# Optimization experiments

Measured on AMD Instinct MI355X. Metric: run time of the kernel, lower is better.

Reference implementation:

```python
import jax, jax.numpy as jnp
import numpy as np

L, D, H, FFN, V = 24, 512, 16, 2048, 1025
HD = D // H
TOP_K = 15
REP_PEN = 1.35


def _layernorm(x, w, b, eps=1e-5):
    m = jnp.mean(x, -1, keepdims=True)
    var = jnp.var(x, -1, keepdims=True)
    return (x - m) / jnp.sqrt(var + eps) * w + b


def _sine_pe(T, d):
    pos = jnp.arange(T, dtype=jnp.float32)[:, None]
    div = jnp.exp(jnp.arange(0, d, 2, dtype=jnp.float32) * (-np.log(10000.0) / d))
    pe = jnp.zeros((T, d), jnp.float32)
    pe = pe.at[:, 0::2].set(jnp.sin(pos * div))
    pe = pe.at[:, 1::2].set(jnp.cos(pos * div))
    return pe


def setup_inputs():
    S, Ty, B = 2047, 1535, 1
    key = jax.random.key(0)
    ks = jax.random.split(key, 16)
    n = lambda i, sh, s=0.02: jax.random.normal(ks[i], sh, jnp.float32) * s
    return {
        "y": jax.random.randint(ks[0], (B, Ty + 1), 0, V, jnp.int32),
        "k": n(1, (L, S, B, D), 1.0),
        "v": n(2, (L, S, B, D), 1.0),
        "y_emb": n(3, (B, Ty, D), 1.0),
        "x_example": n(4, (B, 512), 1.0),
        "alpha": jnp.ones((1,), jnp.float32),
        "emb_table": n(5, (V, D)),
        "in_proj_w": n(6, (L, 3 * D, D)),
        "in_proj_b": jnp.zeros((L, 3 * D), jnp.float32),
        "out_w": n(7, (L, D, D)),
        "out_b": jnp.zeros((L, D), jnp.float32),
        "ln1_w": jnp.ones((L, D), jnp.float32),
        "ln1_b": jnp.zeros((L, D), jnp.float32),
        "ln2_w": jnp.ones((L, D), jnp.float32),
        "ln2_b": jnp.zeros((L, D), jnp.float32),
        "ffn_w1": n(8, (L, FFN, D)),
        "ffn_b1": jnp.zeros((L, FFN), jnp.float32),
        "ffn_w2": n(9, (L, D, FFN)),
        "ffn_b2": jnp.zeros((L, D), jnp.float32),
        "pred_w": n(10, (V, D)),
        "pred_b": jnp.zeros((V,), jnp.float32),
        "noise": jax.random.normal(ks[11], (V,), jnp.float32),
    }


def reference(y, k, v, y_emb, x_example, alpha, emb_table,
              in_proj_w, in_proj_b, out_w, out_b,
              ln1_w, ln1_b, ln2_w, ln2_b,
              ffn_w1, ffn_b1, ffn_w2, ffn_b2,
              pred_w, pred_b, noise):
    B = y.shape[0]
    # pad KV caches by one slot along seq dim (dim 1) -> [L, S+1, B, D]
    k_pad = jnp.pad(k, ((0, 0), (0, 1), (0, 0), (0, 0)))
    v_pad = jnp.pad(v, ((0, 0), (0, 1), (0, 0), (0, 0)))

    # embed newest token, extend y_emb cache
    new_emb = emb_table[y[:, -1:]]                       # [B,1,D]
    y_emb_new = jnp.concatenate([y_emb, new_emb], axis=1)  # [B,T,D]
    T = y_emb_new.shape[1]
    pe = _sine_pe(T, D)
    y_pos = y_emb_new + alpha * pe[None]                 # scale=False -> x_scale=1
    x = y_pos[:, -1:]                                    # [B,1,D] single query token

    scale = 1.0 / jnp.sqrt(jnp.float32(HD))

    def scan_body(x, per):
        kl, vl, wqkv, bqkv, wo, bo, g1, b1, g2, b2, fw1, fb1, fw2, fb2 = per
        qkv = jnp.einsum('bqd,ed->bqe', x, wqkv) + bqkv  # [B,1,3D]
        q, k_new, v_new = jnp.split(qkv, 3, axis=-1)
        kl = kl.at[-1].set(k_new[:, 0])                  # write into last cache slot
        vl = vl.at[-1].set(v_new[:, 0])
        qh = q.reshape(B, 1, H, HD)
        kh = kl.reshape(-1, B, H, HD)                    # [S+1,B,H,hd]
        vh = vl.reshape(-1, B, H, HD)
        scores = jnp.einsum('bqhd,sbhd->bhqs', qh, kh) * scale
        attn = jax.nn.softmax(scores, axis=-1)
        ctx = jnp.einsum('bhqs,sbhd->bqhd', attn, vh).reshape(B, 1, D)
        attn_out = jnp.einsum('bqd,ed->bqe', ctx, wo) + bo
        x = _layernorm(x + attn_out, g1, b1)             # post-LN (torch default)
        hdn = jax.nn.relu(jnp.einsum('bqd,fd->bqf', x, fw1) + fb1)
        ff = jnp.einsum('bqf,df->bqd', hdn, fw2) + fb2
        x = _layernorm(x + ff, g2, b2)
        return x, (kl, vl)

    x, (k_out, v_out) = jax.lax.scan(
        scan_body, x,
        (k_pad, v_pad, in_proj_w, in_proj_b, out_w, out_b,
         ln1_w, ln1_b, ln2_w, ln2_b, ffn_w1, ffn_b1, ffn_w2, ffn_b2))

    logits = jnp.einsum('bd,vd->bv', x[:, -1], pred_w) + pred_b  # [B,V]

    # ---- sampling on logits[0] ----
    lg = logits[0]
    prev = y[0]
    # repetition penalty (gather -> transform -> scatter; dup indices write same value)
    score = lg[prev]
    score = jnp.where(score < 0, score * REP_PEN, score / REP_PEN)
    lg = lg.at[prev].set(score)
    # top_p == 1.0 -> skipped; temperature == 1.0
    pivot = jax.lax.top_k(lg, TOP_K)[0][-1]
    lg = jnp.where(lg < pivot, -jnp.inf, lg)
    probs = jax.nn.softmax(lg)
    # faithful to source: argmax(probs / randn_like(probs))
    samples = jnp.argmax(probs / noise).astype(jnp.int32)[None, None]  # [1,1]
    y_new = jnp.concatenate([y, samples.astype(y.dtype)], axis=1)
    return y_new, k_out, v_out, y_emb_new, logits, samples
```

## Files before the change

### kernel.cpp

```cpp
#include <hip/hip_runtime.h>
#include <math.h>

#define LL 24
#define DD 512
#define HH 16
#define FFD 2048
#define VV 1025
#define SS 2047
#define TKV 2048
#define TYY 1535
#define NBLK 256
#define NT 512

constexpr size_t O_YNEW  = 0;
constexpr size_t O_KOUT  = 1537;
constexpr size_t O_VOUT  = O_KOUT + (size_t)LL*TKV*DD;
constexpr size_t O_YEMB  = O_VOUT + (size_t)LL*TKV*DD;
constexpr size_t O_LOGITS= O_YEMB + (size_t)(TYY+1)*DD;
constexpr size_t O_SAMP  = O_LOGITS + VV;

constexpr int W_FFA  = 0;
constexpr int W_WY   = 8192;
constexpr int W_PART = 16384;
constexpr int W_KN   = 25088;
constexpr int W_VN   = 25600;

struct P {
  const int* y; const float* k; const float* v; const float* yemb;
  const float* alpha; const float* emb;
  const float* ipw; const float* ipb; const float* ow; const float* ob;
  const float* l1w; const float* l1b; const float* l2w; const float* l2b;
  const float* f1w; const float* f1b; const float* f2w; const float* f2b;
  const float* pw; const float* pb; const float* noise;
  float* out; float* ws;
};

__device__ __forceinline__ float dot4(float4 a, float4 b){
  return a.x*b.x + a.y*b.y + a.z*b.z + a.w*b.w;
}
__device__ __forceinline__ float ldv(const float* pp){
  return __hip_atomic_load(pp, __ATOMIC_RELAXED, __HIP_MEMORY_SCOPE_AGENT);
}
__device__ __forceinline__ void stv(float* pp, float v){
  __hip_atomic_store(pp, v, __ATOMIC_RELAXED, __HIP_MEMORY_SCOPE_AGENT);
}
__device__ __forceinline__ unsigned ldu(const unsigned* pp){
  return __hip_atomic_load(pp, __ATOMIC_RELAXED, __HIP_MEMORY_SCOPE_AGENT);
}

__device__ __forceinline__ void lbar(){
  asm volatile("s_waitcnt lgkmcnt(0)" ::: "memory");
  __builtin_amdgcn_s_barrier();
  __builtin_amdgcn_sched_barrier(0);
}

__device__ __forceinline__ void barr_arrive(unsigned* flags, unsigned ph){
  asm volatile("s_waitcnt vmcnt(0) lgkmcnt(0)" ::: "memory");
  __builtin_amdgcn_s_barrier();
  __builtin_amdgcn_sched_barrier(0);
  if (threadIdx.x == 0)
    __hip_atomic_store(&flags[blockIdx.x*16], ph, __ATOMIC_RELAXED, __HIP_MEMORY_SCOPE_AGENT);
}
__device__ __forceinline__ void barr_wait(unsigned* flags, unsigned ph){
  const int t = threadIdx.x;
  if (t < 64){
    for (;;){
      int ok = 1;
      #pragma unroll
      for (int i=0;i<4;++i) ok &= (int)(ldu(&flags[(t*4+i)*16]) >= ph);
      if (__all(ok)) break;
    }
  }
  __builtin_amdgcn_s_barrier();
  asm volatile("" ::: "memory");
}
__device__ __forceinline__ void barr_wait_head(unsigned* flags, unsigned ph, int h){
  const int t = threadIdx.x;
  if (t < 64){
    for (;;){
      int ok = 1;
      if (t < 16) ok = (int)(ldu(&flags[(t*16 + h)*16]) >= ph);
      if (__all(ok)) break;
    }
  }
  __builtin_amdgcn_s_barrier();
  asm volatile("" ::: "memory");
}

__device__ __forceinline__ float2 bsum2(float a, float b2, float2* r8, int t){
  for (int off=32; off; off>>=1){ a += __shfl_xor(a, off); b2 += __shfl_xor(b2, off); }
  lbar();
  if ((t & 63) == 0) r8[t >> 6] = make_float2(a, b2);
  lbar();
  float2 s = r8[0];
  #pragma unroll
  for (int i=1;i<8;++i){ s.x += r8[i].x; s.y += r8[i].y; }
  return s;
}
__device__ __forceinline__ void ln512g(float r, float g, float bb,
                                       float* dst, float2* r8, int t)
{
  float2 s = bsum2(r, r*r, r8, t);
  float mean = s.x * (1.f/512.f);
  float var  = fmaxf(s.y * (1.f/512.f) - mean*mean, 0.f);
  dst[t] = (r - mean) * rsqrtf(var + 1e-5f) * g + bb;
}
__device__ __forceinline__ void bargmax(float v, int i, float* r8v, int* r8i,
                                        int t, float& ov, int& oi)
{
  for (int off=32; off; off>>=1){
    float v2 = __shfl_xor(v, off); int i2 = __shfl_xor(i, off);
    if (v2 > v || (v2 == v && i2 < i)){ v = v2; i = i2; }
  }
  lbar();
  if ((t & 63) == 0){ r8v[t>>6] = v; r8i[t>>6] = i; }
  lbar();
  ov = r8v[0]; oi = r8i[0];
  #pragma unroll
  for (int kk=1; kk<8; ++kk){
    float v2 = r8v[kk]; int i2 = r8i[kk];
    if (v2 > ov || (v2 == ov && i2 < oi)){ ov = v2; oi = i2; }
  }
}

struct RegsQ  { float4 w[8]; float b[4]; };
struct RegsKV { float4 k0,k1,v0,v1; };
struct RegsTl { float4 t0,t1; float bias; };
struct RegsLN { float g2,b2,fb2; };
struct RegsBC { float2 oww; float4 f1p0,f1p1,f2p0,f2p1;
                float g1,b1,obv,f1bv; };

__device__ __forceinline__ void issueQ(const P& p, int l, int h, int t, RegsQ& q){
  const int lane = t & 63, w = t >> 6;
  const float* Wb = p.ipw + (size_t)l*1536*DD;
  const float* Bb = p.ipb + (size_t)l*1536;
  #pragma unroll
  for (int pp=0; pp<4; ++pp){
    int row = h*32 + w + 8*pp;
    const float4* wr = (const float4*)(Wb + (size_t)row*DD);
    q.w[2*pp] = wr[lane]; q.w[2*pp+1] = wr[lane+64];
    q.b[pp] = Bb[row];
  }
}
__device__ __forceinline__ void issueL(const P& p, int b, int t, RegsQ& q){
  const int lane = t & 63, w = t >> 6;
  int row = (w < 4) ? b*4 + w : ((b == 255 && w == 4) ? 1024 : -1);
  if (row >= 0){
    const float4* wr = (const float4*)(p.pw + (size_t)row*DD);
    q.w[0] = wr[lane]; q.w[1] = wr[lane+64];
    q.b[0] = p.pb[row];
  }
}
__device__ __forceinline__ void issueKV(const P& p, int l, int h, int c, int t,
                                        RegsKV& kv){
  const float* kb = p.k + (size_t)l*SS*DD;
  const float* vb = p.v + (size_t)l*SS*DD;
  const int s0 = c*128;
  kv.k0 = kv.v0 = kv.k1 = kv.v1 = make_float4(0,0,0,0);
  {
    int row = t >> 3, c4 = (t & 7)*4, s = s0 + row;
    if (s < SS){
      kv.k0 = *(const float4*)&kb[(size_t)s*DD + h*32 + c4];
      kv.v0 = *(const float4*)&vb[(size_t)s*DD + h*32 + c4];
    }
  }
  {
    int idx = t + NT;
    int row = idx >> 3, c4 = (idx & 7)*4, s = s0 + row;
    if (s < SS){
      kv.k1 = *(const float4*)&kb[(size_t)s*DD + h*32 + c4];
      kv.v1 = *(const float4*)&vb[(size_t)s*DD + h*32 + c4];
    }
  }
}
__device__ __forceinline__ void issueTl(const P& p, int l, int h, int c, int t,
                                        RegsTl& tl){
  const int lane = t & 63, w = t >> 6;
  if (w < 4){
    int isv = w >> 1;
    int row = 512 + isv*512 + h*32 + c*2 + (w&1);
    const float4* wr = (const float4*)(p.ipw + (size_t)l*1536*DD + (size_t)row*DD);
    tl.t0 = wr[lane]; tl.t1 = wr[lane+64];
    tl.bias = p.ipb[(size_t)l*1536 + row];
  }
}
__device__ __forceinline__ void issueLN(const P& p, int l, int t, RegsLN& r){
  r.g2 = p.l2w[(size_t)l*DD + t];
  r.b2 = p.l2b[(size_t)l*DD + t];
  r.fb2= p.f2b[(size_t)l*DD + t];
}
__device__ __forceinline__ void issueBC(const P& p, int l, int b, int h, int c,
                                        int t, RegsBC& bc){
  const int lane = t & 63, w = t >> 6;
  bc.oww = *(const float2*)(p.ow + (size_t)l*DD*DD
            + (size_t)(c*32 + (t>>4))*DD + h*32 + (t&15)*2);
  {
    int f = b*8 + w;
    const float4* wr = (const float4*)(p.f1w + (size_t)l*FFD*DD + (size_t)f*DD);
    bc.f1p0 = wr[lane]; bc.f1p1 = wr[lane+64];
    bc.f1bv = p.f1b[(size_t)l*FFD + f];
  }
  {
    const float* wr = p.f2w + (size_t)l*DD*FFD + (size_t)t*FFD + b*8;
    bc.f2p0 = *(const float4*)wr;
    bc.f2p1 = *(const float4*)(wr+4);
  }
  bc.g1  = p.l1w[(size_t)l*DD + t];
  bc.b1  = p.l1b[(size_t)l*DD + t];
  bc.obv = p.ob[(size_t)l*DD + t];
}

__global__ __launch_bounds__(NT, 1) void mega_kernel(P p)
{
  __shared__ __align__(16) float S_kl[128*33];
  __shared__ __align__(16) float S_vl[128*33];
  __shared__ __align__(16) float S_x[512];
  __shared__ float S_ps[128];
  __shared__ float S_cacc[512];
  __shared__ float S_pb[544];
  __shared__ float S_q[32];
  __shared__ float S_kn[32];
  __shared__ float S_vn[32];
  __shared__ float S_ctx[32];
  __shared__ float S_scal[4];
  __shared__ float S_hdn[8];
  __shared__ float2 S_r82[8];
  __shared__ float S_r8v[8];
  __shared__ int   S_r8i[8];

  const int t = threadIdx.x, b = blockIdx.x;
  const int lane = t & 63, w = t >> 6;
  const int h = b & 15, c = b >> 4;
  unsigned* flags = (unsigned*)p.ws;
  float* wsd = p.ws + 4352;
  float* out = p.out;
  unsigned ph = 0;

  RegsQ q; RegsKV kv; RegsTl tl; RegsLN lnp; RegsBC bc;
  issueQ(p, 0, h, t, q);
  issueKV(p, 0, h, c, t, kv);
  issueTl(p, 0, h, c, t, tl);

  for (int l = 0; l < LL; ++l){
    float fs = 0.f;
    if (l > 0){
      const float* fb = wsd + W_FFA + (size_t)((l+1)&1)*4096;
      #pragma unroll
      for (int i=0;i<8;++i) fs += ldv(&fb[i*512 + t]);
    }
    issueBC(p, l, b, h, c, t, bc);

    if (l == 0){
      int tok = p.y[1535];
      float a0 = p.alpha[0];
      float ev = p.emb[(size_t)tok*DD + t];
      float ang = 1535.0f * expf((float)(2*(t>>1)) * (-9.210340371976184f/512.0f));
      float pe = (t & 1) ? cosf(ang) : sinf(ang);
      S_x[t] = ev + a0*pe;
      if (b == 0) for (int i=t;i<1536;i+=NT)
        __builtin_nontemporal_store((float)p.y[i], out + O_YNEW + i);
      if (b == 1)
        __builtin_nontemporal_store(ev, out + O_YEMB + (size_t)TYY*DD + t);
      lbar();
    } else {
      float r = S_x[t] + lnp.fb2 + fs;
      ln512g(r, lnp.g2, lnp.b2, S_x, S_r82, t);
      lbar();
    }

    #pragma unroll
    for (int pp=0; pp<4; ++pp){
      float s = dot4(q.w[2*pp],   ((const float4*)S_x)[lane])
              + dot4(q.w[2*pp+1], ((const float4*)S_x)[lane+64]);
      for (int off=32; off; off>>=1) s += __shfl_xor(s, off);
      if (lane == 0) S_q[w + 8*pp] = s + q.b[pp];
    }
    if (w < 4){
      int isv = w >> 1;
      int col = h*32 + c*2 + (w & 1);
      float s = dot4(tl.t0, ((const float4*)S_x)[lane])
              + dot4(tl.t1, ((const float4*)S_x)[lane+64]);
      for (int off=32; off; off>>=1) s += __shfl_xor(s, off);
      if (lane == 0){
        float val = s + tl.bias;
        stv(&wsd[(isv ? W_VN : W_KN) + col], val);
        __builtin_nontemporal_store(val,
          out + (isv ? O_VOUT : O_KOUT) + (size_t)l*TKV*DD + (size_t)SS*DD + col);
      }
    }
    {
      int r0 = t >> 3, c40 = (t & 7)*4;
      int lb = r0*33 + c40;
      S_kl[lb+0]=kv.k0.x; S_kl[lb+1]=kv.k0.y; S_kl[lb+2]=kv.k0.z; S_kl[lb+3]=kv.k0.w;
      S_vl[lb+0]=kv.v0.x; S_vl[lb+1]=kv.v0.y; S_vl[lb+2]=kv.v0.z; S_vl[lb+3]=kv.v0.w;
      int idx = t + NT;
      int r1 = idx >> 3, c41 = (idx & 7)*4;
      int lb1 = r1*33 + c41;
      S_kl[lb1+0]=kv.k1.x; S_kl[lb1+1]=kv.k1.y; S_kl[lb1+2]=kv.k1.z; S_kl[lb1+3]=kv.k1.w;
      S_vl[lb1+0]=kv.v1.x; S_vl[lb1+1]=kv.v1.y; S_vl[lb1+2]=kv.v1.z; S_vl[lb1+3]=kv.v1.w;
    }
    lbar();

    {
      const int s0 = c*128;
      float pv = 0.f;
      if (t < 128 && (s0 + t) < SS){
        float acc = 0.f;
        #pragma unroll
        for (int j=0;j<32;++j) acc += S_kl[t*33+j]*S_q[j];
        pv = expf(acc * 0.17677669529663687f);
      }
      if (t < 128) S_ps[t] = pv;
      lbar();
      int g = t >> 5, j = t & 31;
      float ca = 0.f;
      #pragma unroll
      for (int i=0;i<8;++i){ int r = g*8+i; ca += S_ps[r]*S_vl[r*33+j]; }
      S_cacc[g*32 + j] = ca;
      lbar();
      float* pbase = wsd + W_PART + (size_t)(h*16+c)*34;
      if (t < 32){
        float v2 = 0.f;
        #pragma unroll
        for (int gg=0; gg<16; ++gg) v2 += S_cacc[gg*32 + t];
        stv(&pbase[t], v2);
      } else if (t >= 64 && t < 128){
        int ll2 = t - 64;
        float dv = S_ps[ll2] + S_ps[ll2+64];
        for (int off=32; off; off>>=1) dv += __shfl_xor(dv, off);
        if (ll2 == 0) stv(&pbase[32], dv);
      }
    }
    barr_arrive(flags, ++ph);
    {
      const int s0 = c*128;
      float* ko = out + O_KOUT + (size_t)l*TKV*DD;
      float* vo = out + O_VOUT + (size_t)l*TKV*DD;
      {
        int row = t >> 3, c4 = (t & 7)*4, s = s0 + row;
        if (s < SS){
          size_t go = (size_t)s*DD + h*32 + c4;
          __builtin_nontemporal_store(kv.k0.x, ko+go);
          __builtin_nontemporal_store(kv.k0.y, ko+go+1);
          __builtin_nontemporal_store(kv.k0.z, ko+go+2);
          __builtin_nontemporal_store(kv.k0.w, ko+go+3);
          __builtin_nontemporal_store(kv.v0.x, vo+go);
          __builtin_nontemporal_store(kv.v0.y, vo+go+1);
          __builtin_nontemporal_store(kv.v0.z, vo+go+2);
          __builtin_nontemporal_store(kv.v0.w, vo+go+3);
        }
      }
      {
        int idx = t + NT;
        int row = idx >> 3, c4 = (idx & 7)*4, s = s0 + row;
        if (s < SS){
          size_t go = (size_t)s*DD + h*32 + c4;
          __builtin_nontemporal_store(kv.k1.x, ko+go);
          __builtin_nontemporal_store(kv.k1.y, ko+go+1);
          __builtin_nontemporal_store(kv.k1.z, ko+go+2);
          __builtin_nontemporal_store(kv.k1.w, ko+go+3);
          __builtin_nontemporal_store(kv.v1.x, vo+go);
          __builtin_nontemporal_store(kv.v1.y, vo+go+1);
          __builtin_nontemporal_store(kv.v1.z, vo+go+2);
          __builtin_nontemporal_store(kv.v1.w, vo+go+3);
        }
      }
    }
    barr_wait_head(flags, ph, h);

    {
      for (int i=t; i<544; i+=NT) S_pb[i] = ldv(&wsd[W_PART + h*544 + i]);
      if (t < 32){ S_kn[t] = ldv(&wsd[W_KN + h*32 + t]); S_vn[t] = ldv(&wsd[W_VN + h*32 + t]); }
      lbar();
      if (t < 32){
        float tsp = S_q[t] * S_kn[t];
        for (int off=16; off; off>>=1) tsp += __shfl_xor(tsp, off, 32);
        if (t == 0){
          float et = expf(tsp * 0.17677669529663687f);
          float den = et;
          #pragma unroll
          for (int cc=0; cc<16; ++cc) den += S_pb[cc*34+32];
          S_scal[0] = et; S_scal[1] = den;
        }
      }
      lbar();
      if (t < 32){
        float cv = S_scal[0] * S_vn[t];
        #pragma unroll
        for (int cc=0; cc<16; ++cc) cv += S_pb[cc*34 + t];
        S_ctx[t] = cv / S_scal[1];
      }
      lbar();
      int j2 = (t & 15) * 2;
      float s = bc.oww.x*S_ctx[j2] + bc.oww.y*S_ctx[j2+1];
      s += __shfl_xor(s, 8, 16); s += __shfl_xor(s, 4, 16);
      s += __shfl_xor(s, 2, 16); s += __shfl_xor(s, 1, 16);
      if ((t & 15) == 0) stv(&wsd[W_WY + h*512 + c*32 + (t>>4)], s);
    }
    barr_arrive(flags, ++ph);
    if (l < 23){
      issueKV(p, l+1, h, c, t, kv);
      issueTl(p, l+1, h, c, t, tl);
    }
    issueLN(p, l, t, lnp);
    barr_wait(flags, ph);

    {
      float xs = 0.f;
      #pragma unroll
      for (int i=0;i<16;++i) xs += ldv(&wsd[W_WY + i*512 + t]);
      float r = S_x[t] + bc.obv + xs;
      ln512g(r, bc.g1, bc.b1, S_x, S_r82, t);
      lbar();
      {
        float s = dot4(bc.f1p0, ((const float4*)S_x)[lane])
                + dot4(bc.f1p1, ((const float4*)S_x)[lane+64]);
        for (int off=32; off; off>>=1) s += __shfl_xor(s, off);
        if (lane == 0) S_hdn[w] = fmaxf(s + bc.f1bv, 0.f);
      }
      lbar();
      float con = bc.f2p0.x*S_hdn[0]+bc.f2p0.y*S_hdn[1]
                + bc.f2p0.z*S_hdn[2]+bc.f2p0.w*S_hdn[3]
                + bc.f2p1.x*S_hdn[4]+bc.f2p1.y*S_hdn[5]
                + bc.f2p1.z*S_hdn[6]+bc.f2p1.w*S_hdn[7];
      atomicAdd(&wsd[W_FFA + (size_t)(l&1)*4096 + (size_t)(b&7)*512 + t], con);
      if (t < 16) stv(&wsd[W_FFA + (size_t)((l+1)&1)*4096 + b*16 + t], 0.f);
    }
    barr_arrive(flags, ++ph);
    if (l < 23) issueQ(p, l+1, h, t, q);
    else        issueL(p, b, t, q);
    barr_wait(flags, ph);
  }

  {
    float fs = 0.f;
    const float* fb = wsd + W_FFA + (size_t)((LL-1)&1)*4096;
    #pragma unroll
    for (int i=0;i<8;++i) fs += ldv(&fb[i*512 + t]);
    float r = S_x[t] + lnp.fb2 + fs;
    ln512g(r, lnp.g2, lnp.b2, S_x, S_r82, t);
    lbar();
    if (w < 4 || (b == 255 && w == 4)){
      int row = (w < 4) ? b*4 + w : 1024;
      float s = dot4(q.w[0], ((const float4*)S_x)[lane])
              + dot4(q.w[1], ((const float4*)S_x)[lane+64]);
      for (int off=32; off; off>>=1) s += __shfl_xor(s, off);
      if (lane == 0) stv(&out[O_LOGITS+row], s + q.b[0]);
    }
  }
  barr_arrive(flags, ++ph);
  barr_wait(flags, ph);

  if (b == 0){
    float* lg  = S_kl;
    float* lgc = S_kl + 1025;
    int*   pen = (int*)(S_kl + 2050);
    for (int i=t;i<VV;i+=NT){ lg[i] = ldv(&out[O_LOGITS+i]); pen[i]=0; }
    lbar();
    for (int i=t;i<1536;i+=NT) pen[p.y[i]] = 1;
    lbar();
    for (int i=t;i<VV;i+=NT){
      if (pen[i]){ float s = lg[i]; lg[i] = (s<0.f) ? s*1.35f : s/1.35f; }
    }
    lbar();
    for (int i=t;i<VV;i+=NT) lgc[i]=lg[i];
    lbar();
    float sM = 0.f, sPiv = 0.f;
    for (int it=0; it<15; ++it){
      float bv = -INFINITY; int bi = VV;
      for (int i=t;i<VV;i+=NT){ float v2=lgc[i]; if (v2>bv){bv=v2;bi=i;} }
      float ov; int oi;
      bargmax(bv, bi, S_r8v, S_r8i, t, ov, oi);
      if (it==0)  sM   = ov;
      if (it==14) sPiv = ov;
      if (t==0) lgc[oi] = -INFINITY;
      lbar();
    }
    float zl = 0.f;
    for (int i=t;i<VV;i+=NT){
      float lv = lg[i];
      float pv2 = (lv < sPiv) ? 0.f : expf(lv - sM);
      lgc[i] = pv2; zl += pv2;
    }
    {
      float2 s = bsum2(zl, 0.f, S_r82, t);
      zl = s.x;
    }
    lbar();
    float bv=-INFINITY; int bi=VV;
    for (int i=t;i<VV;i+=NT){
      float val = (lgc[i]/zl)/p.noise[i];
      if (val>bv){bv=val;bi=i;}
    }
    float ov; int oi;
    bargmax(bv, bi, S_r8v, S_r8i, t, ov, oi);
    if (t==0){
      float sf = (float)oi;
      out[O_SAMP] = sf;
      out[O_YNEW+1536] = sf;
    }
  } else {
    const int nf4 = (TYY*DD)/4;
    for (int qq = (b-1)*NT + t; qq < nf4; qq += 255*NT){
      float4 vq = *(const float4*)&p.yemb[qq*4];
      float* dq = out + O_YEMB + (size_t)qq*4;
      __builtin_nontemporal_store(vq.x, dq);
      __builtin_nontemporal_store(vq.y, dq+1);
      __builtin_nontemporal_store(vq.z, dq+2);
      __builtin_nontemporal_store(vq.w, dq+3);
    }
  }
}

extern "C" void kernel_launch(void* const* d_in, const int* in_sizes, int n_in,
                              void* d_out, int out_size, void* d_ws, size_t ws_size,
                              hipStream_t stream)
{
  P p;
  p.y    = (const int*)d_in[0];
  p.k    = (const float*)d_in[1];
  p.v    = (const float*)d_in[2];
  p.yemb = (const float*)d_in[3];
  p.alpha= (const float*)d_in[5];
  p.emb  = (const float*)d_in[6];
  p.ipw  = (const float*)d_in[7];
  p.ipb  = (const float*)d_in[8];
  p.ow   = (const float*)d_in[9];
  p.ob   = (const float*)d_in[10];
  p.l1w  = (const float*)d_in[11];
  p.l1b  = (const float*)d_in[12];
  p.l2w  = (const float*)d_in[13];
  p.l2b  = (const float*)d_in[14];
  p.f1w  = (const float*)d_in[15];
  p.f1b  = (const float*)d_in[16];
  p.f2w  = (const float*)d_in[17];
  p.f2b  = (const float*)d_in[18];
  p.pw   = (const float*)d_in[19];
  p.pb   = (const float*)d_in[20];
  p.noise= (const float*)d_in[21];
  p.out  = (float*)d_out;
  p.ws   = (float*)d_ws;

  hipMemsetAsync(d_ws, 0, 50176, stream);
  void* args[] = { &p };
  hipLaunchCooperativeKernel((void*)mega_kernel, dim3(NBLK), dim3(NT), args, 0, stream);
}
```

Measured before the change: 455.3 us.

## Vectorize misaligned KV/y_emb output stores and widen FFN atomic accumulation buffers

The output buffer starts at offset 1537, so the K/V and y_emb copies previously wrote scalar nontemporal stores. These are now realigned into 16-byte vector stores using lane shuffles for K/V and overlapping float4 loads for y_emb, with scalar stores for the ragged edges. FFN second-layer atomics are spread over 16 accumulation slots instead of 8 to reduce atomic contention, at the cost of more reads when summing them. The weight prefetches (issueBC split) are moved to later barrier phases to shorten the register live range and overlap the loads with other work.

```diff
diff --git a/kernel.cpp b/kernel.cpp
--- a/kernel.cpp
+++ b/kernel.cpp
@@ -12,6 +12,8 @@
 #define NBLK 256
 #define NT 512
 
+typedef float f4v __attribute__((ext_vector_type(4)));
+
 constexpr size_t O_YNEW  = 0;
 constexpr size_t O_KOUT  = 1537;
 constexpr size_t O_VOUT  = O_KOUT + (size_t)LL*TKV*DD;
@@ -20,10 +22,10 @@
 constexpr size_t O_SAMP  = O_LOGITS + VV;
 
 constexpr int W_FFA  = 0;
-constexpr int W_WY   = 8192;
-constexpr int W_PART = 16384;
-constexpr int W_KN   = 25088;
-constexpr int W_VN   = 25600;
+constexpr int W_WY   = 16384;
+constexpr int W_PART = 24576;
+constexpr int W_KN   = 33280;
+constexpr int W_VN   = 33792;
 
 struct P {
   const int* y; const float* k; const float* v; const float* yemb;
@@ -53,7 +55,6 @@
   __builtin_amdgcn_s_barrier();
   __builtin_amdgcn_sched_barrier(0);
 }
-
 __device__ __forceinline__ void barr_arrive(unsigned* flags, unsigned ph){
   asm volatile("s_waitcnt vmcnt(0) lgkmcnt(0)" ::: "memory");
   __builtin_amdgcn_s_barrier();
@@ -189,8 +190,8 @@
   r.b2 = p.l2b[(size_t)l*DD + t];
   r.fb2= p.f2b[(size_t)l*DD + t];
 }
-__device__ __forceinline__ void issueBC(const P& p, int l, int b, int h, int c,
-                                        int t, RegsBC& bc){
+__device__ __forceinline__ void issueBC1(const P& p, int l, int b, int h,
+                                         int c, int t, RegsBC& bc){
   const int lane = t & 63, w = t >> 6;
   bc.oww = *(const float2*)(p.ow + (size_t)l*DD*DD
             + (size_t)(c*32 + (t>>4))*DD + h*32 + (t&15)*2);
@@ -200,14 +201,40 @@
     bc.f1p0 = wr[lane]; bc.f1p1 = wr[lane+64];
     bc.f1bv = p.f1b[(size_t)l*FFD + f];
   }
-  {
-    const float* wr = p.f2w + (size_t)l*DD*FFD + (size_t)t*FFD + b*8;
-    bc.f2p0 = *(const float4*)wr;
-    bc.f2p1 = *(const float4*)(wr+4);
-  }
   bc.g1  = p.l1w[(size_t)l*DD + t];
   bc.b1  = p.l1b[(size_t)l*DD + t];
   bc.obv = p.ob[(size_t)l*DD + t];
+}
+__device__ __forceinline__ void issueBC2(const P& p, int l, int b, int t,
+                                         RegsBC& bc){
+  const float* wr = p.f2w + (size_t)l*DD*FFD + (size_t)t*FFD + b*8;
+  bc.f2p0 = *(const float4*)wr;
+  bc.f2p1 = *(const float4*)(wr+4);
+}
+
+__device__ __forceinline__ void copy_row(float* ko, float* vo,
+    float4 kk, float4 vv, int s, int j, int h){
+  float nkx = __shfl_down(kk.x, 1), nky = __shfl_down(kk.y, 1), nkz = __shfl_down(kk.z, 1);
+  float nvx = __shfl_down(vv.x, 1), nvy = __shfl_down(vv.y, 1), nvz = __shfl_down(vv.z, 1);
+  if (s < SS){
+    size_t go = (size_t)s*DD + h*32;
+    if (j < 7){
+      f4v kf = {kk.w, nkx, nky, nkz};
+      f4v vf = {vv.w, nvx, nvy, nvz};
+      __builtin_nontemporal_store(kf, (f4v*)(ko + go + 3 + 4*j));
+      __builtin_nontemporal_store(vf, (f4v*)(vo + go + 3 + 4*j));
+    }
+    if (j == 0){
+      __builtin_nontemporal_store(kk.x, ko+go);   __builtin_nontemporal_store(kk.y, ko+go+1);
+      __builtin_nontemporal_store(kk.z, ko+go+2);
+      __builtin_nontemporal_store(vv.x, vo+go);   __builtin_nontemporal_store(vv.y, vo+go+1);
+      __builtin_nontemporal_store(vv.z, vo+go+2);
+    }
+    if (j == 7){
+      __builtin_nontemporal_store(kk.w, ko+go+31);
+      __builtin_nontemporal_store(vv.w, vo+go+31);
+    }
+  }
 }
 
 __global__ __launch_bounds__(NT, 1) void mega_kernel(P p)
@@ -244,12 +271,10 @@
   for (int l = 0; l < LL; ++l){
     float fs = 0.f;
     if (l > 0){
-      const float* fb = wsd + W_FFA + (size_t)((l+1)&1)*4096;
+      const float* fb = wsd + W_FFA + (size_t)((l+1)&1)*8192;
       #pragma unroll
-      for (int i=0;i<8;++i) fs += ldv(&fb[i*512 + t]);
-    }
-    issueBC(p, l, b, h, c, t, bc);
-
+      for (int i=0;i<16;++i) fs += ldv(&fb[i*512 + t]);
+    }
     if (l == 0){
       int tok = p.y[1535];
       float a0 = p.alpha[0];
@@ -332,39 +357,14 @@
       }
     }
     barr_arrive(flags, ++ph);
+    issueBC1(p, l, b, h, c, t, bc);
     {
       const int s0 = c*128;
       float* ko = out + O_KOUT + (size_t)l*TKV*DD;
       float* vo = out + O_VOUT + (size_t)l*TKV*DD;
-      {
-        int row = t >> 3, c4 = (t & 7)*4, s = s0 + row;
-        if (s < SS){
-          size_t go = (size_t)s*DD + h*32 + c4;
-          __builtin_nontemporal_store(kv.k0.x, ko+go);
-          __builtin_nontemporal_store(kv.k0.y, ko+go+1);
-          __builtin_nontemporal_store(kv.k0.z, ko+go+2);
-          __builtin_nontemporal_store(kv.k0.w, ko+go+3);
-          __builtin_nontemporal_store(kv.v0.x, vo+go);
-          __builtin_nontemporal_store(kv.v0.y, vo+go+1);
-          __builtin_nontemporal_store(kv.v0.z, vo+go+2);
-          __builtin_nontemporal_store(kv.v0.w, vo+go+3);
-        }
-      }
-      {
-        int idx = t + NT;
-        int row = idx >> 3, c4 = (idx & 7)*4, s = s0 + row;
-        if (s < SS){
-          size_t go = (size_t)s*DD + h*32 + c4;
-          __builtin_nontemporal_store(kv.k1.x, ko+go);
-          __builtin_nontemporal_store(kv.k1.y, ko+go+1);
-          __builtin_nontemporal_store(kv.k1.z, ko+go+2);
-          __builtin_nontemporal_store(kv.k1.w, ko+go+3);
-          __builtin_nontemporal_store(kv.v1.x, vo+go);
-          __builtin_nontemporal_store(kv.v1.y, vo+go+1);
-          __builtin_nontemporal_store(kv.v1.z, vo+go+2);
-          __builtin_nontemporal_store(kv.v1.w, vo+go+3);
-        }
-      }
+      int j = t & 7;
+      copy_row(ko, vo, kv.k0, kv.v0, s0 + (t>>3), j, h);
+      copy_row(ko, vo, kv.k1, kv.v1, s0 + ((t+NT)>>3), j, h);
     }
     barr_wait_head(flags, ph, h);
 
@@ -398,6 +398,7 @@
       if ((t & 15) == 0) stv(&wsd[W_WY + h*512 + c*32 + (t>>4)], s);
     }
     barr_arrive(flags, ++ph);
+    issueBC2(p, l, b, t, bc);
     if (l < 23){
       issueKV(p, l+1, h, c, t, kv);
       issueTl(p, l+1, h, c, t, tl);
@@ -423,8 +424,8 @@
                 + bc.f2p0.z*S_hdn[2]+bc.f2p0.w*S_hdn[3]
                 + bc.f2p1.x*S_hdn[4]+bc.f2p1.y*S_hdn[5]
                 + bc.f2p1.z*S_hdn[6]+bc.f2p1.w*S_hdn[7];
-      atomicAdd(&wsd[W_FFA + (size_t)(l&1)*4096 + (size_t)(b&7)*512 + t], con);
-      if (t < 16) stv(&wsd[W_FFA + (size_t)((l+1)&1)*4096 + b*16 + t], 0.f);
+      atomicAdd(&wsd[W_FFA + (size_t)(l&1)*8192 + (size_t)(b&15)*512 + t], con);
+      if (t < 32) stv(&wsd[W_FFA + (size_t)((l+1)&1)*8192 + b*32 + t], 0.f);
     }
     barr_arrive(flags, ++ph);
     if (l < 23) issueQ(p, l+1, h, t, q);
@@ -434,9 +435,9 @@
 
   {
     float fs = 0.f;
-    const float* fb = wsd + W_FFA + (size_t)((LL-1)&1)*4096;
+    const float* fb = wsd + W_FFA + (size_t)((LL-1)&1)*8192;
     #pragma unroll
-    for (int i=0;i<8;++i) fs += ldv(&fb[i*512 + t]);
+    for (int i=0;i<16;++i) fs += ldv(&fb[i*512 + t]);
     float r = S_x[t] + lnp.fb2 + fs;
     ln512g(r, lnp.g2, lnp.b2, S_x, S_r82, t);
     lbar();
@@ -500,14 +501,16 @@
       out[O_YNEW+1536] = sf;
     }
   } else {
-    const int nf4 = (TYY*DD)/4;
+    const int nf4 = (TYY*DD - 4)/4;
     for (int qq = (b-1)*NT + t; qq < nf4; qq += 255*NT){
-      float4 vq = *(const float4*)&p.yemb[qq*4];
-      float* dq = out + O_YEMB + (size_t)qq*4;
-      __builtin_nontemporal_store(vq.x, dq);
-      __builtin_nontemporal_store(vq.y, dq+1);
-      __builtin_nontemporal_store(vq.z, dq+2);
-      __builtin_nontemporal_store(vq.w, dq+3);
+      float4 a = *(const float4*)&p.yemb[qq*4];
+      float4 bq = *(const float4*)&p.yemb[qq*4 + 4];
+      f4v o = {a.w, bq.x, bq.y, bq.z};
+      __builtin_nontemporal_store(o, (f4v*)(out + O_YEMB + 3 + (size_t)qq*4));
+    }
+    if (b == 1){
+      if (t < 3) __builtin_nontemporal_store(p.yemb[t], out + O_YEMB + t);
+      if (t == 3) __builtin_nontemporal_store(p.yemb[TYY*DD-1], out + O_YEMB + TYY*DD - 1);
     }
   }
 }
@@ -541,7 +544,7 @@
   p.out  = (float*)d_out;
   p.ws   = (float*)d_ws;
 
-  hipMemsetAsync(d_ws, 0, 50176, stream);
+  hipMemsetAsync(d_ws, 0, 82944, stream);
   void* args[] = { &p };
   hipLaunchCooperativeKernel((void*)mega_kernel, dim3(NBLK), dim3(NT), args, 0, stream);
 }
```

Result: slower. 499.2 us (+9.6%).

## Replace per-chunk attention partials with atomic accumulation and parallelize QK dot

Applied to the files above, without the earlier changes.

Attention partial numerators and denominators are now accumulated with global atomicAdd into double-buffered slots instead of being stored per chunk and summed by each head's blocks. The out-projection partials are atomically reduced into 4 slots instead of 16, which cuts the reads in the post-barrier reduction. The QK score computation is spread across all 512 threads, four lanes per row, instead of 128. This shortens the serial reads on the critical path after each grid barrier. In exchange it adds atomic contention, extra zeroing stores for the next-parity buffers, and a larger workspace memset.

```diff
diff --git a/kernel.cpp b/kernel.cpp
--- a/kernel.cpp
+++ b/kernel.cpp
@@ -12,6 +12,8 @@
 #define NBLK 256
 #define NT 512
 
+typedef float f4v __attribute__((ext_vector_type(4)));
+
 constexpr size_t O_YNEW  = 0;
 constexpr size_t O_KOUT  = 1537;
 constexpr size_t O_VOUT  = O_KOUT + (size_t)LL*TKV*DD;
@@ -19,11 +21,12 @@
 constexpr size_t O_LOGITS= O_YEMB + (size_t)(TYY+1)*DD;
 constexpr size_t O_SAMP  = O_LOGITS + VV;
 
-constexpr int W_FFA  = 0;
-constexpr int W_WY   = 8192;
-constexpr int W_PART = 16384;
-constexpr int W_KN   = 25088;
-constexpr int W_VN   = 25600;
+constexpr int W_X1A = 0;
+constexpr int W_FFA = 4096;
+constexpr int W_NUM = 12288;
+constexpr int W_DEN = 13312;
+constexpr int W_KN  = 13824;
+constexpr int W_VN  = 14336;
 
 struct P {
   const int* y; const float* k; const float* v; const float* yemb;
@@ -53,7 +56,6 @@
   __builtin_amdgcn_s_barrier();
   __builtin_amdgcn_sched_barrier(0);
 }
-
 __device__ __forceinline__ void barr_arrive(unsigned* flags, unsigned ph){
   asm volatile("s_waitcnt vmcnt(0) lgkmcnt(0)" ::: "memory");
   __builtin_amdgcn_s_barrier();
@@ -217,8 +219,8 @@
   __shared__ __align__(16) float S_x[512];
   __shared__ float S_ps[128];
   __shared__ float S_cacc[512];
-  __shared__ float S_pb[544];
   __shared__ float S_q[32];
+  __shared__ float S_num[32];
   __shared__ float S_kn[32];
   __shared__ float S_vn[32];
   __shared__ float S_ctx[32];
@@ -242,9 +244,10 @@
   issueTl(p, 0, h, c, t, tl);
 
   for (int l = 0; l < LL; ++l){
+    const int par = l & 1, np = (l+1) & 1;
     float fs = 0.f;
     if (l > 0){
-      const float* fb = wsd + W_FFA + (size_t)((l+1)&1)*4096;
+      const float* fb = wsd + W_FFA + (size_t)np*4096;
       #pragma unroll
       for (int i=0;i<8;++i) fs += ldv(&fb[i*512 + t]);
     }
@@ -303,14 +306,16 @@
 
     {
       const int s0 = c*128;
-      float pv = 0.f;
-      if (t < 128 && (s0 + t) < SS){
+      {
+        int row = t >> 2, d0 = (t & 3) * 8;
         float acc = 0.f;
         #pragma unroll
-        for (int j=0;j<32;++j) acc += S_kl[t*33+j]*S_q[j];
-        pv = expf(acc * 0.17677669529663687f);
-      }
-      if (t < 128) S_ps[t] = pv;
+        for (int j=0;j<8;++j) acc += S_kl[row*33 + d0 + j] * S_q[d0 + j];
+        acc += __shfl_xor(acc, 1, 4);
+        acc += __shfl_xor(acc, 2, 4);
+        if ((t & 3) == 0)
+          S_ps[row] = ((s0 + row) < SS) ? expf(acc * 0.17677669529663687f) : 0.f;
+      }
       lbar();
       int g = t >> 5, j = t & 31;
       float ca = 0.f;
@@ -318,17 +323,16 @@
       for (int i=0;i<8;++i){ int r = g*8+i; ca += S_ps[r]*S_vl[r*33+j]; }
       S_cacc[g*32 + j] = ca;
       lbar();
-      float* pbase = wsd + W_PART + (size_t)(h*16+c)*34;
       if (t < 32){
         float v2 = 0.f;
         #pragma unroll
         for (int gg=0; gg<16; ++gg) v2 += S_cacc[gg*32 + t];
-        stv(&pbase[t], v2);
+        atomicAdd(&wsd[W_NUM + par*512 + h*32 + t], v2);
       } else if (t >= 64 && t < 128){
         int ll2 = t - 64;
         float dv = S_ps[ll2] + S_ps[ll2+64];
         for (int off=32; off; off>>=1) dv += __shfl_xor(dv, off);
-        if (ll2 == 0) stv(&pbase[32], dv);
+        if (ll2 == 0) atomicAdd(&wsd[W_DEN + par*256 + h*16], dv);
       }
     }
     barr_arrive(flags, ++ph);
@@ -369,33 +373,33 @@
     barr_wait_head(flags, ph, h);
 
     {
-      for (int i=t; i<544; i+=NT) S_pb[i] = ldv(&wsd[W_PART + h*544 + i]);
-      if (t < 32){ S_kn[t] = ldv(&wsd[W_KN + h*32 + t]); S_vn[t] = ldv(&wsd[W_VN + h*32 + t]); }
+      if (t < 32){
+        S_num[t] = ldv(&wsd[W_NUM + par*512 + h*32 + t]);
+        S_kn[t]  = ldv(&wsd[W_KN + h*32 + t]);
+        S_vn[t]  = ldv(&wsd[W_VN + h*32 + t]);
+      }
+      if (t == 64) S_scal[1] = ldv(&wsd[W_DEN + par*256 + h*16]);
+      if (t < 2) stv(&wsd[W_NUM + np*512 + b*2 + t], 0.f);
+      if (b < 16 && t == 96) stv(&wsd[W_DEN + np*256 + b*16], 0.f);
       lbar();
       if (t < 32){
         float tsp = S_q[t] * S_kn[t];
         for (int off=16; off; off>>=1) tsp += __shfl_xor(tsp, off, 32);
         if (t == 0){
           float et = expf(tsp * 0.17677669529663687f);
-          float den = et;
-          #pragma unroll
-          for (int cc=0; cc<16; ++cc) den += S_pb[cc*34+32];
-          S_scal[0] = et; S_scal[1] = den;
+          S_scal[0] = et;
+          S_scal[2] = S_scal[1] + et;
         }
       }
       lbar();
-      if (t < 32){
-        float cv = S_scal[0] * S_vn[t];
-        #pragma unroll
-        for (int cc=0; cc<16; ++cc) cv += S_pb[cc*34 + t];
-        S_ctx[t] = cv / S_scal[1];
-      }
+      if (t < 32) S_ctx[t] = (S_num[t] + S_scal[0]*S_vn[t]) / S_scal[2];
       lbar();
       int j2 = (t & 15) * 2;
       float s = bc.oww.x*S_ctx[j2] + bc.oww.y*S_ctx[j2+1];
       s += __shfl_xor(s, 8, 16); s += __shfl_xor(s, 4, 16);
       s += __shfl_xor(s, 2, 16); s += __shfl_xor(s, 1, 16);
-      if ((t & 15) == 0) stv(&wsd[W_WY + h*512 + c*32 + (t>>4)], s);
+      if ((t & 15) == 0)
+        atomicAdd(&wsd[W_X1A + par*2048 + (h&3)*512 + c*32 + (t>>4)], s);
     }
     barr_arrive(flags, ++ph);
     if (l < 23){
@@ -406,10 +410,11 @@
     barr_wait(flags, ph);
 
     {
-      float xs = 0.f;
-      #pragma unroll
-      for (int i=0;i<16;++i) xs += ldv(&wsd[W_WY + i*512 + t]);
-      float r = S_x[t] + bc.obv + xs;
+      float x0 = ldv(&wsd[W_X1A + par*2048       + t]);
+      float x1 = ldv(&wsd[W_X1A + par*2048 +  512 + t]);
+      float x2 = ldv(&wsd[W_X1A + par*2048 + 1024 + t]);
+      float x3 = ldv(&wsd[W_X1A + par*2048 + 1536 + t]);
+      float r = S_x[t] + bc.obv + x0 + x1 + x2 + x3;
       ln512g(r, bc.g1, bc.b1, S_x, S_r82, t);
       lbar();
       {
@@ -423,8 +428,9 @@
                 + bc.f2p0.z*S_hdn[2]+bc.f2p0.w*S_hdn[3]
                 + bc.f2p1.x*S_hdn[4]+bc.f2p1.y*S_hdn[5]
                 + bc.f2p1.z*S_hdn[6]+bc.f2p1.w*S_hdn[7];
-      atomicAdd(&wsd[W_FFA + (size_t)(l&1)*4096 + (size_t)(b&7)*512 + t], con);
-      if (t < 16) stv(&wsd[W_FFA + (size_t)((l+1)&1)*4096 + b*16 + t], 0.f);
+      atomicAdd(&wsd[W_FFA + (size_t)par*4096 + (size_t)(b&7)*512 + t], con);
+      if (t < 16) stv(&wsd[W_FFA + (size_t)np*4096 + b*16 + t], 0.f);
+      if (t < 8)  stv(&wsd[W_X1A + (size_t)np*2048 + b*8 + t], 0.f);
     }
     barr_arrive(flags, ++ph);
     if (l < 23) issueQ(p, l+1, h, t, q);
@@ -541,7 +547,7 @@
   p.out  = (float*)d_out;
   p.ws   = (float*)d_ws;
 
-  hipMemsetAsync(d_ws, 0, 50176, stream);
+  hipMemsetAsync(d_ws, 0, 76800, stream);
   void* args[] = { &p };
   hipLaunchCooperativeKernel((void*)mega_kernel, dim3(NBLK), dim3(NT), args, 0, stream);
 }
```

New measurement: 444.4 us, median of 2. 1.02x faster.
